# Kernel tuning notes

Measured on AMD Instinct MI355X. Metric: run time of the kernel, lower is better.

Reference implementation:

```python
import jax, jax.numpy as jnp
import numpy as np

NUM_USERS = 100000
NUM_ITEMS = 50000
NUM_EDGES = 1000000
HIDDEN = 128


def setup_inputs() -> dict:
    key = jax.random.key(0)
    ks = jax.random.split(key, 8)
    z_user = jax.random.normal(ks[0], (NUM_USERS, HIDDEN), dtype=jnp.float32)
    z_item = jax.random.normal(ks[1], (NUM_ITEMS, HIDDEN), dtype=jnp.float32)
    row_idx = jax.random.randint(ks[2], (NUM_EDGES,), 0, NUM_USERS, dtype=jnp.int64 if jax.config.jax_enable_x64 else jnp.int32)
    col_idx = jax.random.randint(ks[3], (NUM_EDGES,), 0, NUM_ITEMS, dtype=jnp.int64 if jax.config.jax_enable_x64 else jnp.int32)
    # Linear params (PyTorch Linear: y = x @ W.T + b); store as [in, out] for einsum.
    scale1 = 1.0 / np.sqrt(2 * HIDDEN)
    scale2 = 1.0 / np.sqrt(HIDDEN)
    W1 = jax.random.uniform(ks[4], (2 * HIDDEN, HIDDEN), jnp.float32, -scale1, scale1)
    b1 = jax.random.uniform(ks[5], (HIDDEN,), jnp.float32, -scale1, scale1)
    W2 = jax.random.uniform(ks[6], (HIDDEN, 1), jnp.float32, -scale2, scale2)
    b2 = jax.random.uniform(ks[7], (1,), jnp.float32, -scale2, scale2)
    return {"z_user": z_user, "z_item": z_item, "row_idx": row_idx,
            "col_idx": col_idx, "W1": W1, "b1": b1, "W2": W2, "b2": b2}


def reference(z_user, z_item, row_idx, col_idx, W1, b1, W2, b2):
    # Gather endpoint embeddings for each candidate edge: [E, H] each.
    zu = z_user[row_idx]
    zi = z_item[col_idx]
    # Equivalent to concat([zu, zi]) @ W1 without materializing the concat:
    h = zu @ W1[:HIDDEN] + zi @ W1[HIDDEN:] + b1  # [E, H]
    h = jax.nn.relu(h)
    out = h @ W2 + b2  # [E, 1]
    return out
```

## Files before the change

kernel.cpp:

```cpp
#include <hip/hip_runtime.h>
#include <hip/hip_bf16.h>
#include <stdint.h>

#define H 128
#define NU 100000
#define NI 50000

typedef __attribute__((ext_vector_type(8))) short short8;
typedef __attribute__((ext_vector_type(4))) float f32x4;

__device__ __forceinline__ uint16_t f2bf(float f) {
    uint32_t x = __float_as_uint(f);
    return (uint16_t)((x + 0x7fffu + ((x >> 16) & 1u)) >> 16);
}
__device__ __forceinline__ uint32_t cvtpk(float lo, float hi) {
    uint32_t r;
    asm("v_cvt_pk_bf16_f32 %0, %1, %2" : "=v"(r) : "v"(lo), "v"(hi));
    return r;
}
__device__ __forceinline__ float cvt_ub0(uint32_t v) { float f; asm("v_cvt_f32_ubyte0 %0, %1" : "=v"(f) : "v"(v)); return f; }
__device__ __forceinline__ float cvt_ub1(uint32_t v) { float f; asm("v_cvt_f32_ubyte1 %0, %1" : "=v"(f) : "v"(v)); return f; }
__device__ __forceinline__ float cvt_ub2(uint32_t v) { float f; asm("v_cvt_f32_ubyte2 %0, %1" : "=v"(f) : "v"(v)); return f; }
__device__ __forceinline__ float cvt_ub3(uint32_t v) { float f; asm("v_cvt_f32_ubyte3 %0, %1" : "=v"(f) : "v"(v)); return f; }

__device__ __forceinline__ int lds_off(int row, int k) {
    return (row * 256 + k * 2) ^ ((row & 7) << 4);
}


__global__ __launch_bounds__(256) void wconv_kernel(
    const float* __restrict__ W1, uint16_t* __restrict__ Wt)
{
    __shared__ char lds[32768];
    const int half = blockIdx.x;
    const float* W = W1 + (size_t)half * H * H;
    uint16_t* Out = Wt + (size_t)half * H * H;
    const int tid = threadIdx.x;

    int n4 = (tid & 31) * 4;
    int k  = tid >> 5;
    #pragma unroll
    for (int p = 0; p < 16; ++p, k += 8) {
        f32x4 v = *(const f32x4*)(W + (size_t)k * H + n4);
        *(uint16_t*)(lds + lds_off(n4 + 0, k)) = f2bf(v.x);
        *(uint16_t*)(lds + lds_off(n4 + 1, k)) = f2bf(v.y);
        *(uint16_t*)(lds + lds_off(n4 + 2, k)) = f2bf(v.z);
        *(uint16_t*)(lds + lds_off(n4 + 3, k)) = f2bf(v.w);
    }
    __syncthreads();
    int n = tid >> 1;
    #pragma unroll
    for (int p = 0; p < 8; ++p) {
        int chunk = (tid & 1) * 8 + p;
        uint4 v = *(const uint4*)(lds + lds_off(n, chunk * 8));
        *(uint4*)(Out + (size_t)n * H + chunk * 8) = v;
    }
}

__global__ __launch_bounds__(256) void proj_kernel(
    const float* __restrict__ z_user, const float* __restrict__ z_item,
    const uint16_t* __restrict__ Wt, const float* __restrict__ b1,
    uint8_t* __restrict__ U8, uint8_t* __restrict__ I8,
    float* __restrict__ Us, float* __restrict__ Is, int nub)
{
    __shared__ char lds[32768];

    int bid = blockIdx.x;
    const float* Z; const uint16_t* Wth; uint8_t* Out8; float* Sc; int M; bool addb1;
    if (bid < nub) { Z = z_user; Wth = Wt;         Out8 = U8; Sc = Us; M = NU; addb1 = false; }
    else { bid -= nub; Z = z_item; Wth = Wt + H*H; Out8 = I8; Sc = Is; M = NI; addb1 = true; }
    const int row0 = bid * 128;
    const int tid = threadIdx.x;

    {
        int n = tid >> 1;
        #pragma unroll
        for (int p = 0; p < 8; ++p) {
            int chunk = (tid & 1) * 8 + p;
            uint4 v = *(const uint4*)(Wth + (size_t)n * H + chunk * 8);
            *(uint4*)(lds + lds_off(n, chunk * 8)) = v;
        }
    }
    __syncthreads();

    const int w  = tid >> 6;
    const int l  = tid & 63;
    const int lr = l & 15;
    const int lk = (l >> 4) * 8;

    int r0 = row0 + w * 32 + lr;
    int r1 = r0 + 16;
    const float* a0p = Z + (size_t)(r0 < M ? r0 : M - 1) * H;
    const float* a1p = Z + (size_t)(r1 < M ? r1 : M - 1) * H;

    f32x4 acc[2][8];
    #pragma unroll
    for (int m0 = 0; m0 < 2; ++m0)
        #pragma unroll
        for (int n0 = 0; n0 < 8; ++n0)
            acc[m0][n0] = (f32x4){0.f, 0.f, 0.f, 0.f};

    #pragma unroll
    for (int kk = 0; kk < 4; ++kk) {
        int kb = kk * 32 + lk;
        f32x4 v00 = *(const f32x4*)(a0p + kb);
        f32x4 v01 = *(const f32x4*)(a0p + kb + 4);
        f32x4 v10 = *(const f32x4*)(a1p + kb);
        f32x4 v11 = *(const f32x4*)(a1p + kb + 4);
        short8 a0, a1;
        uint32_t* A0 = (uint32_t*)&a0;
        uint32_t* A1 = (uint32_t*)&a1;
        A0[0] = cvtpk(v00.x, v00.y); A0[1] = cvtpk(v00.z, v00.w);
        A0[2] = cvtpk(v01.x, v01.y); A0[3] = cvtpk(v01.z, v01.w);
        A1[0] = cvtpk(v10.x, v10.y); A1[1] = cvtpk(v10.z, v10.w);
        A1[2] = cvtpk(v11.x, v11.y); A1[3] = cvtpk(v11.z, v11.w);
        #pragma unroll
        for (int n0 = 0; n0 < 8; ++n0) {
            short8 b = *(const short8*)(lds + lds_off(n0*16 + lr, kb));
            acc[0][n0] = __builtin_amdgcn_mfma_f32_16x16x32_bf16(a0, b, acc[0][n0], 0, 0, 0);
            acc[1][n0] = __builtin_amdgcn_mfma_f32_16x16x32_bf16(a1, b, acc[1][n0], 0, 0, 0);
        }
    }

    float b1v[8];
    #pragma unroll
    for (int n0 = 0; n0 < 8; ++n0) b1v[n0] = addb1 ? b1[n0*16 + lr] : 0.f;

    const int rbase = row0 + w * 32;
    #pragma unroll
    for (int m0 = 0; m0 < 2; ++m0) {
        #pragma unroll
        for (int ri = 0; ri < 4; ++ri) {
            int gr = rbase + m0*16 + (l >> 4) * 4 + ri;
            float v[8];
            float am = 0.f;
            #pragma unroll
            for (int n0 = 0; n0 < 8; ++n0) {
                v[n0] = acc[m0][n0][ri] + b1v[n0];
                am = fmaxf(am, fabsf(v[n0]));
            }
            am = fmaxf(am, __shfl_xor(am, 1));
            am = fmaxf(am, __shfl_xor(am, 2));
            am = fmaxf(am, __shfl_xor(am, 4));
            am = fmaxf(am, __shfl_xor(am, 8));
            float s = am * (1.0f / 127.0f);
            float r = 127.0f / fmaxf(am, 1e-30f);
            uint32_t lo = 0, hi = 0;
            #pragma unroll
            for (int n0 = 0; n0 < 4; ++n0) {
                uint32_t q8 = (uint32_t)fmaf(v[n0], r, 128.5f);
                lo |= q8 << (8 * n0);
            }
            #pragma unroll
            for (int n0 = 4; n0 < 8; ++n0) {
                uint32_t q8 = (uint32_t)fmaf(v[n0], r, 128.5f);
                hi |= q8 << (8 * (n0 - 4));
            }
            if (gr < M) {
                *(uint2*)(Out8 + (size_t)gr * H + lr * 8) = make_uint2(lo, hi);
                if (lr == 0) Sc[gr] = s;
            }
        }
    }
}

__device__ __forceinline__ float edge_dot8(uint2 u, uint2 i, float su, float si,
                                           const float* w2v) {
    float k = -128.0f * (su + si);
    float acc = 0.f, h;
    h = fmaf(su, cvt_ub0(u.x), fmaf(si, cvt_ub0(i.x), k)); acc = fmaf(fmaxf(h, 0.f), w2v[0], acc);
    h = fmaf(su, cvt_ub1(u.x), fmaf(si, cvt_ub1(i.x), k)); acc = fmaf(fmaxf(h, 0.f), w2v[1], acc);
    h = fmaf(su, cvt_ub2(u.x), fmaf(si, cvt_ub2(i.x), k)); acc = fmaf(fmaxf(h, 0.f), w2v[2], acc);
    h = fmaf(su, cvt_ub3(u.x), fmaf(si, cvt_ub3(i.x), k)); acc = fmaf(fmaxf(h, 0.f), w2v[3], acc);
    h = fmaf(su, cvt_ub0(u.y), fmaf(si, cvt_ub0(i.y), k)); acc = fmaf(fmaxf(h, 0.f), w2v[4], acc);
    h = fmaf(su, cvt_ub1(u.y), fmaf(si, cvt_ub1(i.y), k)); acc = fmaf(fmaxf(h, 0.f), w2v[5], acc);
    h = fmaf(su, cvt_ub2(u.y), fmaf(si, cvt_ub2(i.y), k)); acc = fmaf(fmaxf(h, 0.f), w2v[6], acc);
    h = fmaf(su, cvt_ub3(u.y), fmaf(si, cvt_ub3(i.y), k)); acc = fmaf(fmaxf(h, 0.f), w2v[7], acc);
    return acc;
}

__device__ __forceinline__ float group_reduce(float acc) {
    acc += __shfl_xor(acc, 8);
    acc += __shfl_xor(acc, 4);
    acc += __shfl_xor(acc, 2);
    acc += __shfl_xor(acc, 1);
    return acc;
}

__global__ __launch_bounds__(256) void edge_kernel(
    const uint8_t* __restrict__ U8, const uint8_t* __restrict__ I8,
    const float* __restrict__ Us, const float* __restrict__ Is,
    const int* __restrict__ row_idx, const int* __restrict__ col_idx,
    const float* __restrict__ W2, const float* __restrict__ b2p,
    float* __restrict__ out, int E)
{
    const int l = threadIdx.x & 63;
    const int g = l >> 4;
    const int t = l & 15;

    float w2v[8];
    #pragma unroll
    for (int j = 0; j < 8; ++j) w2v[j] = W2[j * 16 + t];
    const float b2 = *b2p;

    const int wid = (int)((blockIdx.x * blockDim.x + threadIdx.x) >> 6);
    const int nw  = (int)((gridDim.x * blockDim.x) >> 6);
    const int stride = nw * 16;
    const int Emain = E & ~3;

    for (int e0 = wid * 16 + g * 4; e0 + 3 < E; e0 += stride) {
        int4 rp = *(const int4*)(row_idx + e0);
        int4 cp = *(const int4*)(col_idx + e0);
        uint2 u0 = *(const uint2*)(U8 + (size_t)rp.x * H + t * 8);
        uint2 i0 = *(const uint2*)(I8 + (size_t)cp.x * H + t * 8);
        uint2 u1 = *(const uint2*)(U8 + (size_t)rp.y * H + t * 8);
        uint2 i1 = *(const uint2*)(I8 + (size_t)cp.y * H + t * 8);
        uint2 u2 = *(const uint2*)(U8 + (size_t)rp.z * H + t * 8);
        uint2 i2 = *(const uint2*)(I8 + (size_t)cp.z * H + t * 8);
        uint2 u3 = *(const uint2*)(U8 + (size_t)rp.w * H + t * 8);
        uint2 i3 = *(const uint2*)(I8 + (size_t)cp.w * H + t * 8);
        float su0 = Us[rp.x], si0 = Is[cp.x];
        float su1 = Us[rp.y], si1 = Is[cp.y];
        float su2 = Us[rp.z], si2 = Is[cp.z];
        float su3 = Us[rp.w], si3 = Is[cp.w];
        float a0 = group_reduce(edge_dot8(u0, i0, su0, si0, w2v));
        float a1 = group_reduce(edge_dot8(u1, i1, su1, si1, w2v));
        float a2 = group_reduce(edge_dot8(u2, i2, su2, si2, w2v));
        float a3 = group_reduce(edge_dot8(u3, i3, su3, si3, w2v));
        if (t == 0) {
            f32x4 o; o.x = a0 + b2; o.y = a1 + b2; o.z = a2 + b2; o.w = a3 + b2;
            *(f32x4*)(out + e0) = o;
        }
    }
    if (wid == 0 && g == 0) {
        for (int e = Emain; e < E; ++e) {
            int r = row_idx[e], c = col_idx[e];
            uint2 uv = *(const uint2*)(U8 + (size_t)r * H + t * 8);
            uint2 iv = *(const uint2*)(I8 + (size_t)c * H + t * 8);
            float acc = group_reduce(edge_dot8(uv, iv, Us[r], Is[c], w2v));
            if (t == 0) out[e] = acc + b2;
        }
    }
}

extern "C" void kernel_launch(void* const* d_in, const int* in_sizes, int n_in,
                              void* d_out, int out_size, void* d_ws, size_t ws_size,
                              hipStream_t stream) {
    const float* z_user = (const float*)d_in[0];
    const float* z_item = (const float*)d_in[1];
    const int*   row_idx = (const int*)d_in[2];
    const int*   col_idx = (const int*)d_in[3];
    const float* W1 = (const float*)d_in[4];
    const float* b1 = (const float*)d_in[5];
    const float* W2 = (const float*)d_in[6];
    const float* b2 = (const float*)d_in[7];
    float* out = (float*)d_out;
    const int E = in_sizes[2];

    uint8_t* U8 = (uint8_t*)d_ws;
    uint8_t* I8 = U8 + (size_t)NU * H;
    float*   Us = (float*)(I8 + (size_t)NI * H);
    float*   Is = Us + NU;
    uint16_t* Wt = (uint16_t*)(Is + NI);

    const int nub = (NU + 127) / 128;
    const int nib = (NI + 127) / 128;
    wconv_kernel<<<2, 256, 0, stream>>>(W1, Wt);
    proj_kernel<<<nub + nib, 256, 0, stream>>>(z_user, z_item, Wt, b1, U8, I8, Us, Is, nub);
    edge_kernel<<<2048, 256, 0, stream>>>(U8, I8, Us, Is, row_idx, col_idx, W2, b2, out, E);
}
```

Measured before the change: 71.89 us.

## Make projection kernel persistent and process eight edges per group

The projection kernel becomes persistent: 512 blocks loop over the 1173 row tiles and restage the bf16 weight half into LDS only when switching between user and item tiles, so fewer blocks each pay for the weight load. The edge kernel now handles 8 edges per 16-lane group instead of 4, issuing more independent gathers before the reductions so more memory latency overlaps. The trade-off is higher register pressure in the edge kernel and possible load imbalance from the fixed grid in the projection.

```diff
diff --git a/kernel.cpp b/kernel.cpp
--- a/kernel.cpp
+++ b/kernel.cpp
@@ -61,104 +61,108 @@
     const float* __restrict__ z_user, const float* __restrict__ z_item,
     const uint16_t* __restrict__ Wt, const float* __restrict__ b1,
     uint8_t* __restrict__ U8, uint8_t* __restrict__ I8,
-    float* __restrict__ Us, float* __restrict__ Is, int nub)
+    float* __restrict__ Us, float* __restrict__ Is, int nub, int ntiles)
 {
     __shared__ char lds[32768];
-
-    int bid = blockIdx.x;
-    const float* Z; const uint16_t* Wth; uint8_t* Out8; float* Sc; int M; bool addb1;
-    if (bid < nub) { Z = z_user; Wth = Wt;         Out8 = U8; Sc = Us; M = NU; addb1 = false; }
-    else { bid -= nub; Z = z_item; Wth = Wt + H*H; Out8 = I8; Sc = Is; M = NI; addb1 = true; }
-    const int row0 = bid * 128;
     const int tid = threadIdx.x;
-
-    {
-        int n = tid >> 1;
-        #pragma unroll
-        for (int p = 0; p < 8; ++p) {
-            int chunk = (tid & 1) * 8 + p;
-            uint4 v = *(const uint4*)(Wth + (size_t)n * H + chunk * 8);
-            *(uint4*)(lds + lds_off(n, chunk * 8)) = v;
-        }
-    }
-    __syncthreads();
-
     const int w  = tid >> 6;
     const int l  = tid & 63;
     const int lr = l & 15;
     const int lk = (l >> 4) * 8;
-
-    int r0 = row0 + w * 32 + lr;
-    int r1 = r0 + 16;
-    const float* a0p = Z + (size_t)(r0 < M ? r0 : M - 1) * H;
-    const float* a1p = Z + (size_t)(r1 < M ? r1 : M - 1) * H;
-
-    f32x4 acc[2][8];
-    #pragma unroll
-    for (int m0 = 0; m0 < 2; ++m0)
-        #pragma unroll
-        for (int n0 = 0; n0 < 8; ++n0)
-            acc[m0][n0] = (f32x4){0.f, 0.f, 0.f, 0.f};
-
-    #pragma unroll
-    for (int kk = 0; kk < 4; ++kk) {
-        int kb = kk * 32 + lk;
-        f32x4 v00 = *(const f32x4*)(a0p + kb);
-        f32x4 v01 = *(const f32x4*)(a0p + kb + 4);
-        f32x4 v10 = *(const f32x4*)(a1p + kb);
-        f32x4 v11 = *(const f32x4*)(a1p + kb + 4);
-        short8 a0, a1;
-        uint32_t* A0 = (uint32_t*)&a0;
-        uint32_t* A1 = (uint32_t*)&a1;
-        A0[0] = cvtpk(v00.x, v00.y); A0[1] = cvtpk(v00.z, v00.w);
-        A0[2] = cvtpk(v01.x, v01.y); A0[3] = cvtpk(v01.z, v01.w);
-        A1[0] = cvtpk(v10.x, v10.y); A1[1] = cvtpk(v10.z, v10.w);
-        A1[2] = cvtpk(v11.x, v11.y); A1[3] = cvtpk(v11.z, v11.w);
-        #pragma unroll
-        for (int n0 = 0; n0 < 8; ++n0) {
-            short8 b = *(const short8*)(lds + lds_off(n0*16 + lr, kb));
-            acc[0][n0] = __builtin_amdgcn_mfma_f32_16x16x32_bf16(a0, b, acc[0][n0], 0, 0, 0);
-            acc[1][n0] = __builtin_amdgcn_mfma_f32_16x16x32_bf16(a1, b, acc[1][n0], 0, 0, 0);
-        }
-    }
-
-    float b1v[8];
-    #pragma unroll
-    for (int n0 = 0; n0 < 8; ++n0) b1v[n0] = addb1 ? b1[n0*16 + lr] : 0.f;
-
-    const int rbase = row0 + w * 32;
-    #pragma unroll
-    for (int m0 = 0; m0 < 2; ++m0) {
-        #pragma unroll
-        for (int ri = 0; ri < 4; ++ri) {
-            int gr = rbase + m0*16 + (l >> 4) * 4 + ri;
-            float v[8];
-            float am = 0.f;
+    int staged = -1;
+
+    for (int tile = blockIdx.x; tile < ntiles; tile += gridDim.x) {
+        int bid = tile;
+        const float* Z; const uint16_t* Wth; uint8_t* Out8; float* Sc; int M; int half;
+        if (bid < nub) { Z = z_user; Wth = Wt;         Out8 = U8; Sc = Us; M = NU; half = 0; }
+        else { bid -= nub; Z = z_item; Wth = Wt + H*H; Out8 = I8; Sc = Is; M = NI; half = 1; }
+        const int row0 = bid * 128;
+
+        if (half != staged) {
+            __syncthreads();
+            int n = tid >> 1;
+            #pragma unroll
+            for (int p = 0; p < 8; ++p) {
+                int chunk = (tid & 1) * 8 + p;
+                uint4 v = *(const uint4*)(Wth + (size_t)n * H + chunk * 8);
+                *(uint4*)(lds + lds_off(n, chunk * 8)) = v;
+            }
+            staged = half;
+            __syncthreads();
+        }
+
+        int r0 = row0 + w * 32 + lr;
+        int r1 = r0 + 16;
+        const float* a0p = Z + (size_t)(r0 < M ? r0 : M - 1) * H;
+        const float* a1p = Z + (size_t)(r1 < M ? r1 : M - 1) * H;
+
+        f32x4 acc[2][8];
+        #pragma unroll
+        for (int m0 = 0; m0 < 2; ++m0)
+            #pragma unroll
+            for (int n0 = 0; n0 < 8; ++n0)
+                acc[m0][n0] = (f32x4){0.f, 0.f, 0.f, 0.f};
+
+        #pragma unroll
+        for (int kk = 0; kk < 4; ++kk) {
+            int kb = kk * 32 + lk;
+            f32x4 v00 = *(const f32x4*)(a0p + kb);
+            f32x4 v01 = *(const f32x4*)(a0p + kb + 4);
+            f32x4 v10 = *(const f32x4*)(a1p + kb);
+            f32x4 v11 = *(const f32x4*)(a1p + kb + 4);
+            short8 a0, a1;
+            uint32_t* A0 = (uint32_t*)&a0;
+            uint32_t* A1 = (uint32_t*)&a1;
+            A0[0] = cvtpk(v00.x, v00.y); A0[1] = cvtpk(v00.z, v00.w);
+            A0[2] = cvtpk(v01.x, v01.y); A0[3] = cvtpk(v01.z, v01.w);
+            A1[0] = cvtpk(v10.x, v10.y); A1[1] = cvtpk(v10.z, v10.w);
+            A1[2] = cvtpk(v11.x, v11.y); A1[3] = cvtpk(v11.z, v11.w);
             #pragma unroll
             for (int n0 = 0; n0 < 8; ++n0) {
-                v[n0] = acc[m0][n0][ri] + b1v[n0];
-                am = fmaxf(am, fabsf(v[n0]));
+                short8 b = *(const short8*)(lds + lds_off(n0*16 + lr, kb));
+                acc[0][n0] = __builtin_amdgcn_mfma_f32_16x16x32_bf16(a0, b, acc[0][n0], 0, 0, 0);
+                acc[1][n0] = __builtin_amdgcn_mfma_f32_16x16x32_bf16(a1, b, acc[1][n0], 0, 0, 0);
             }
-            am = fmaxf(am, __shfl_xor(am, 1));
-            am = fmaxf(am, __shfl_xor(am, 2));
-            am = fmaxf(am, __shfl_xor(am, 4));
-            am = fmaxf(am, __shfl_xor(am, 8));
-            float s = am * (1.0f / 127.0f);
-            float r = 127.0f / fmaxf(am, 1e-30f);
-            uint32_t lo = 0, hi = 0;
-            #pragma unroll
-            for (int n0 = 0; n0 < 4; ++n0) {
-                uint32_t q8 = (uint32_t)fmaf(v[n0], r, 128.5f);
-                lo |= q8 << (8 * n0);
-            }
-            #pragma unroll
-            for (int n0 = 4; n0 < 8; ++n0) {
-                uint32_t q8 = (uint32_t)fmaf(v[n0], r, 128.5f);
-                hi |= q8 << (8 * (n0 - 4));
-            }
-            if (gr < M) {
-                *(uint2*)(Out8 + (size_t)gr * H + lr * 8) = make_uint2(lo, hi);
-                if (lr == 0) Sc[gr] = s;
+        }
+
+        float b1v[8];
+        #pragma unroll
+        for (int n0 = 0; n0 < 8; ++n0) b1v[n0] = half ? b1[n0*16 + lr] : 0.f;
+
+        const int rbase = row0 + w * 32;
+        #pragma unroll
+        for (int m0 = 0; m0 < 2; ++m0) {
+            #pragma unroll
+            for (int ri = 0; ri < 4; ++ri) {
+                int gr = rbase + m0*16 + (l >> 4) * 4 + ri;
+                float v[8];
+                float am = 0.f;
+                #pragma unroll
+                for (int n0 = 0; n0 < 8; ++n0) {
+                    v[n0] = acc[m0][n0][ri] + b1v[n0];
+                    am = fmaxf(am, fabsf(v[n0]));
+                }
+                am = fmaxf(am, __shfl_xor(am, 1));
+                am = fmaxf(am, __shfl_xor(am, 2));
+                am = fmaxf(am, __shfl_xor(am, 4));
+                am = fmaxf(am, __shfl_xor(am, 8));
+                float s = am * (1.0f / 127.0f);
+                float r = 127.0f / fmaxf(am, 1e-30f);
+                uint32_t lo = 0, hi = 0;
+                #pragma unroll
+                for (int n0 = 0; n0 < 4; ++n0) {
+                    uint32_t q8 = (uint32_t)fmaf(v[n0], r, 128.5f);
+                    lo |= q8 << (8 * n0);
+                }
+                #pragma unroll
+                for (int n0 = 4; n0 < 8; ++n0) {
+                    uint32_t q8 = (uint32_t)fmaf(v[n0], r, 128.5f);
+                    hi |= q8 << (8 * (n0 - 4));
+                }
+                if (gr < M) {
+                    *(uint2*)(Out8 + (size_t)gr * H + lr * 8) = make_uint2(lo, hi);
+                    if (lr == 0) Sc[gr] = s;
+                }
             }
         }
     }
@@ -205,31 +209,40 @@
 
     const int wid = (int)((blockIdx.x * blockDim.x + threadIdx.x) >> 6);
     const int nw  = (int)((gridDim.x * blockDim.x) >> 6);
-    const int stride = nw * 16;
-    const int Emain = E & ~3;
-
-    for (int e0 = wid * 16 + g * 4; e0 + 3 < E; e0 += stride) {
-        int4 rp = *(const int4*)(row_idx + e0);
-        int4 cp = *(const int4*)(col_idx + e0);
-        uint2 u0 = *(const uint2*)(U8 + (size_t)rp.x * H + t * 8);
-        uint2 i0 = *(const uint2*)(I8 + (size_t)cp.x * H + t * 8);
-        uint2 u1 = *(const uint2*)(U8 + (size_t)rp.y * H + t * 8);
-        uint2 i1 = *(const uint2*)(I8 + (size_t)cp.y * H + t * 8);
-        uint2 u2 = *(const uint2*)(U8 + (size_t)rp.z * H + t * 8);
-        uint2 i2 = *(const uint2*)(I8 + (size_t)cp.z * H + t * 8);
-        uint2 u3 = *(const uint2*)(U8 + (size_t)rp.w * H + t * 8);
-        uint2 i3 = *(const uint2*)(I8 + (size_t)cp.w * H + t * 8);
-        float su0 = Us[rp.x], si0 = Is[cp.x];
-        float su1 = Us[rp.y], si1 = Is[cp.y];
-        float su2 = Us[rp.z], si2 = Is[cp.z];
-        float su3 = Us[rp.w], si3 = Is[cp.w];
-        float a0 = group_reduce(edge_dot8(u0, i0, su0, si0, w2v));
-        float a1 = group_reduce(edge_dot8(u1, i1, su1, si1, w2v));
-        float a2 = group_reduce(edge_dot8(u2, i2, su2, si2, w2v));
-        float a3 = group_reduce(edge_dot8(u3, i3, su3, si3, w2v));
+    const int stride = nw * 32;
+    const int Emain = E & ~7;
+
+    for (int e0 = wid * 32 + g * 8; e0 + 7 < E; e0 += stride) {
+        int4 ra = *(const int4*)(row_idx + e0);
+        int4 rb = *(const int4*)(row_idx + e0 + 4);
+        int4 ca = *(const int4*)(col_idx + e0);
+        int4 cb = *(const int4*)(col_idx + e0 + 4);
+        int r[8], c[8];
+        r[0]=ra.x; r[1]=ra.y; r[2]=ra.z; r[3]=ra.w;
+        r[4]=rb.x; r[5]=rb.y; r[6]=rb.z; r[7]=rb.w;
+        c[0]=ca.x; c[1]=ca.y; c[2]=ca.z; c[3]=ca.w;
+        c[4]=cb.x; c[5]=cb.y; c[6]=cb.z; c[7]=cb.w;
+
+        uint2 uu[8], ii[8];
+        float su[8], si[8];
+        #pragma unroll
+        for (int q = 0; q < 8; ++q) {
+            uu[q] = *(const uint2*)(U8 + (size_t)r[q] * H + t * 8);
+            ii[q] = *(const uint2*)(I8 + (size_t)c[q] * H + t * 8);
+        }
+        #pragma unroll
+        for (int q = 0; q < 8; ++q) { su[q] = Us[r[q]]; si[q] = Is[c[q]]; }
+
+        float a[8];
+        #pragma unroll
+        for (int q = 0; q < 8; ++q)
+            a[q] = group_reduce(edge_dot8(uu[q], ii[q], su[q], si[q], w2v));
+
         if (t == 0) {
-            f32x4 o; o.x = a0 + b2; o.y = a1 + b2; o.z = a2 + b2; o.w = a3 + b2;
-            *(f32x4*)(out + e0) = o;
+            f32x4 o0; o0.x = a[0] + b2; o0.y = a[1] + b2; o0.z = a[2] + b2; o0.w = a[3] + b2;
+            f32x4 o1; o1.x = a[4] + b2; o1.y = a[5] + b2; o1.z = a[6] + b2; o1.w = a[7] + b2;
+            *(f32x4*)(out + e0)     = o0;
+            *(f32x4*)(out + e0 + 4) = o1;
         }
     }
     if (wid == 0 && g == 0) {
@@ -265,7 +278,8 @@
 
     const int nub = (NU + 127) / 128;
     const int nib = (NI + 127) / 128;
+    const int ntiles = nub + nib;
     wconv_kernel<<<2, 256, 0, stream>>>(W1, Wt);
-    proj_kernel<<<nub + nib, 256, 0, stream>>>(z_user, z_item, Wt, b1, U8, I8, Us, Is, nub);
+    proj_kernel<<<512, 256, 0, stream>>>(z_user, z_item, Wt, b1, U8, I8, Us, Is, nub, ntiles);
     edge_kernel<<<2048, 256, 0, stream>>>(U8, I8, Us, Is, row_idx, col_idx, W2, b2, out, E);
 }
```

Measured after the change: 72.28 us. Within noise of the previous version (+0.6%).

## Software-pipeline edge gathers with double buffering and 8 edges per group

Applied to the files above, without the earlier changes.

Restructures the edge loop so each 16-lane group handles 8 edges per iteration, with gathers for the next iteration and index loads for the one after issued before computing the current one, using ping-pong register buffers. The grid is halved to keep total work per wave balanced. This aims to hide gather latency behind compute, at the cost of much higher register use, which could lower occupancy.

```diff
diff --git a/kernel.cpp b/kernel.cpp
--- a/kernel.cpp
+++ b/kernel.cpp
@@ -187,6 +187,33 @@
     return acc;
 }
 
+#define IDX_LOAD(ra, rb, ca, cb, e) do {              \
+    ra = *(const int4*)(row_idx + (e));               \
+    rb = *(const int4*)(row_idx + (e) + 4);           \
+    ca = *(const int4*)(col_idx + (e));               \
+    cb = *(const int4*)(col_idx + (e) + 4);           \
+} while (0)
+
+#define GATH(uu, ii, su, si, ra, rb, ca, cb) do {                      \
+    int rr_[8] = {ra.x, ra.y, ra.z, ra.w, rb.x, rb.y, rb.z, rb.w};     \
+    int cc_[8] = {ca.x, ca.y, ca.z, ca.w, cb.x, cb.y, cb.z, cb.w};     \
+    _Pragma("unroll") for (int q = 0; q < 8; ++q) {                    \
+        uu[q] = *(const uint2*)(U8 + (size_t)rr_[q] * H + t * 8);      \
+        ii[q] = *(const uint2*)(I8 + (size_t)cc_[q] * H + t * 8); }    \
+    _Pragma("unroll") for (int q = 0; q < 8; ++q) {                    \
+        su[q] = Us[rr_[q]]; si[q] = Is[cc_[q]]; }                      \
+} while (0)
+
+#define COMPUTE(uu, ii, su, si, e) do {                                \
+    float a_[8];                                                       \
+    _Pragma("unroll") for (int q = 0; q < 8; ++q)                      \
+        a_[q] = group_reduce(edge_dot8(uu[q], ii[q], su[q], si[q], w2v)); \
+    if (t == 0) {                                                      \
+        f32x4 o0; o0.x=a_[0]+b2; o0.y=a_[1]+b2; o0.z=a_[2]+b2; o0.w=a_[3]+b2; \
+        f32x4 o1; o1.x=a_[4]+b2; o1.y=a_[5]+b2; o1.z=a_[6]+b2; o1.w=a_[7]+b2; \
+        *(f32x4*)(out + (e)) = o0; *(f32x4*)(out + (e) + 4) = o1; }    \
+} while (0)
+
 __global__ __launch_bounds__(256) void edge_kernel(
     const uint8_t* __restrict__ U8, const uint8_t* __restrict__ I8,
     const float* __restrict__ Us, const float* __restrict__ Is,
@@ -205,35 +232,35 @@
 
     const int wid = (int)((blockIdx.x * blockDim.x + threadIdx.x) >> 6);
     const int nw  = (int)((gridDim.x * blockDim.x) >> 6);
-    const int stride = nw * 16;
-    const int Emain = E & ~3;
-
-    for (int e0 = wid * 16 + g * 4; e0 + 3 < E; e0 += stride) {
-        int4 rp = *(const int4*)(row_idx + e0);
-        int4 cp = *(const int4*)(col_idx + e0);
-        uint2 u0 = *(const uint2*)(U8 + (size_t)rp.x * H + t * 8);
-        uint2 i0 = *(const uint2*)(I8 + (size_t)cp.x * H + t * 8);
-        uint2 u1 = *(const uint2*)(U8 + (size_t)rp.y * H + t * 8);
-        uint2 i1 = *(const uint2*)(I8 + (size_t)cp.y * H + t * 8);
-        uint2 u2 = *(const uint2*)(U8 + (size_t)rp.z * H + t * 8);
-        uint2 i2 = *(const uint2*)(I8 + (size_t)cp.z * H + t * 8);
-        uint2 u3 = *(const uint2*)(U8 + (size_t)rp.w * H + t * 8);
-        uint2 i3 = *(const uint2*)(I8 + (size_t)cp.w * H + t * 8);
-        float su0 = Us[rp.x], si0 = Is[cp.x];
-        float su1 = Us[rp.y], si1 = Is[cp.y];
-        float su2 = Us[rp.z], si2 = Is[cp.z];
-        float su3 = Us[rp.w], si3 = Is[cp.w];
-        float a0 = group_reduce(edge_dot8(u0, i0, su0, si0, w2v));
-        float a1 = group_reduce(edge_dot8(u1, i1, su1, si1, w2v));
-        float a2 = group_reduce(edge_dot8(u2, i2, su2, si2, w2v));
-        float a3 = group_reduce(edge_dot8(u3, i3, su3, si3, w2v));
-        if (t == 0) {
-            f32x4 o; o.x = a0 + b2; o.y = a1 + b2; o.z = a2 + b2; o.w = a3 + b2;
-            *(f32x4*)(out + e0) = o;
+    const int stride = nw * 32;
+    const int e0 = wid * 32 + g * 8;
+    const int niter = (e0 + 7 < E) ? (int)((E - 8 - e0) / stride) + 1 : 0;
+
+    uint2 uuP[8], iiP[8]; float suP[8], siP[8];
+    uint2 uuQ[8], iiQ[8]; float suQ[8], siQ[8];
+    int4 rA0, rA1, cA0, cA1, rB0, rB1, cB0, cB1;
+
+    if (niter > 0) {
+        int e = e0;
+        IDX_LOAD(rA0, rA1, cA0, cA1, e);
+        GATH(uuP, iiP, suP, siP, rA0, rA1, cA0, cA1);
+        if (niter > 1) IDX_LOAD(rB0, rB1, cB0, cB1, e + stride);
+        int n = 0;
+        while (true) {
+            if (n + 1 < niter) GATH(uuQ, iiQ, suQ, siQ, rB0, rB1, cB0, cB1);
+            if (n + 2 < niter) IDX_LOAD(rA0, rA1, cA0, cA1, e + 2 * stride);
+            COMPUTE(uuP, iiP, suP, siP, e);
+            if (++n >= niter) break;
+            e += stride;
+            if (n + 1 < niter) GATH(uuP, iiP, suP, siP, rA0, rA1, cA0, cA1);
+            if (n + 2 < niter) IDX_LOAD(rB0, rB1, cB0, cB1, e + 2 * stride);
+            COMPUTE(uuQ, iiQ, suQ, siQ, e);
+            if (++n >= niter) break;
+            e += stride;
         }
     }
     if (wid == 0 && g == 0) {
-        for (int e = Emain; e < E; ++e) {
+        for (int e = (E & ~7); e < E; ++e) {
             int r = row_idx[e], c = col_idx[e];
             uint2 uv = *(const uint2*)(U8 + (size_t)r * H + t * 8);
             uint2 iv = *(const uint2*)(I8 + (size_t)c * H + t * 8);
@@ -267,5 +294,5 @@
     const int nib = (NI + 127) / 128;
     wconv_kernel<<<2, 256, 0, stream>>>(W1, Wt);
     proj_kernel<<<nub + nib, 256, 0, stream>>>(z_user, z_item, Wt, b1, U8, I8, Us, Is, nub);
-    edge_kernel<<<2048, 256, 0, stream>>>(U8, I8, Us, Is, row_idx, col_idx, W2, b2, out, E);
-}
+    edge_kernel<<<1024, 256, 0, stream>>>(U8, I8, Us, Is, row_idx, col_idx, W2, b2, out, E);
+}
```

New measurement: 77.01 us. 7.1% more time.
